# Optimization experiments

Measured on AMD Instinct MI355X. Metric: run time of the kernel, lower is better.

The kernel has to match this reference:

```python
import jax, jax.numpy as jnp
import numpy as np

N = 100000
E = 1600000
G = 2000
IN_C, HID, OUT = 9, 256, 128
BN_EPS = 1e-5


def setup_inputs() -> dict:
    key = jax.random.key(0)
    ks = jax.random.split(key, 12)
    x = jax.random.normal(ks[0], (N, IN_C), dtype=jnp.float32)
    edge_index = jax.random.randint(ks[1], (2, E), 0, N, dtype=jnp.int64)
    batch = jnp.sort(jax.random.randint(ks[2], (N,), 0, G, dtype=jnp.int64))
    # GCNConv weights (glorot-ish scale) and biases
    W1 = jax.random.normal(ks[3], (IN_C, HID), dtype=jnp.float32) * (1.0 / np.sqrt(IN_C))
    b1 = jnp.zeros((HID,), dtype=jnp.float32)
    W2 = jax.random.normal(ks[4], (HID, OUT), dtype=jnp.float32) * (1.0 / np.sqrt(HID))
    b2 = jnp.zeros((OUT,), dtype=jnp.float32)
    # BatchNorm affine params
    g1 = jnp.ones((HID,), dtype=jnp.float32)
    be1 = jnp.zeros((HID,), dtype=jnp.float32)
    g2 = jnp.ones((OUT,), dtype=jnp.float32)
    be2 = jnp.zeros((OUT,), dtype=jnp.float32)
    return {"x": x, "W1": W1, "b1": b1, "g1": g1, "be1": be1,
            "W2": W2, "b2": b2, "g2": g2, "be2": be2,
            "edge_index": edge_index, "batch": batch}


def _gcn_conv(x, W, b, src, dst, norm):
    # x: [N, F_in] -> [N, F_out]; PyG GCNConv: linear, then normalized scatter-add
    h = x @ W
    msg = h[src] * norm[:, None]                      # [E+N, F_out] edge messages
    out = jax.ops.segment_sum(msg, dst, num_segments=N)
    return out + b


def _batchnorm_train(h, gamma, beta):
    mean = jnp.mean(h, axis=0)
    var = jnp.mean(jnp.square(h - mean), axis=0)      # biased var, as torch BN
    return (h - mean) * jax.lax.rsqrt(var + BN_EPS) * gamma + beta


def reference(x, W1, b1, g1, be1, W2, b2, g2, be2, edge_index, batch):
    src, dst = edge_index[0], edge_index[1]
    loops = jnp.arange(N, dtype=src.dtype)
    src = jnp.concatenate([src, loops])               # add self-loops
    dst = jnp.concatenate([dst, loops])
    deg = jax.ops.segment_sum(jnp.ones_like(dst, dtype=x.dtype), dst, num_segments=N)
    dis = jax.lax.rsqrt(deg)                          # deg >= 1 due to self-loops
    norm = dis[src] * dis[dst]                        # symmetric normalization

    h = _gcn_conv(x, W1, b1, src, dst, norm)
    h = jax.nn.relu(_batchnorm_train(h, g1, be1))
    h = _gcn_conv(h, W2, b2, src, dst, norm)
    h = _batchnorm_train(h, g2, be2)

    # global mean pool over graphs
    sums = jax.ops.segment_sum(h, batch, num_segments=G)
    cnts = jax.ops.segment_sum(jnp.ones((N,), dtype=h.dtype), batch, num_segments=G)
    pooled = sums / jnp.maximum(cnts, 1.0)[:, None]

    # F.normalize(p=2, dim=1)
    nrm = jnp.linalg.norm(pooled, axis=1, keepdims=True)
    return pooled / jnp.maximum(nrm, 1e-12)
```

## Files before the change

kernel.cpp:

```cpp
#include <hip/hip_runtime.h>

#define N_NODES 100000
#define N_EDGES 1600000
#define N_GRAPH 2000
#define INC 9
#define HID 256
#define OUTC 128
#define BN_EPS 1e-5f
#define SCAN_CHUNK 1024
#define NSCAN ((N_NODES + SCAN_CHUNK - 1) / SCAN_CHUNK)
#define SP_NODES 64
#define SP_BLOCKS ((N_NODES + SP_NODES - 1) / SP_NODES)
#define NPART (2 * SP_BLOCKS)

typedef unsigned int uint;
typedef unsigned short ushort;
typedef short bf16x8 __attribute__((ext_vector_type(8)));
typedef float f32x4 __attribute__((ext_vector_type(4)));

static __device__ inline ushort f2bf(float f) {
    uint u = __float_as_uint(f);
    uint r = (u + 0x7fffu + ((u >> 16) & 1u)) >> 16;
    return (ushort)r;
}
static __device__ inline float bflo(uint p) { return __uint_as_float(p << 16); }
static __device__ inline float bfhi(uint p) { return __uint_as_float(p & 0xffff0000u); }


__global__ __launch_bounds__(256) void k_hist(const int* dst, int* degi, int* pose) {
    int e = blockIdx.x * 256 + threadIdx.x;
    if (e < N_EDGES) pose[e] = atomicAdd(&degi[dst[e]], 1);
}

__global__ __launch_bounds__(256) void k_scan1(const int* degi, int* exloc, int* bsum,
                                               float* dis) {
    __shared__ int s[SCAN_CHUNK];
    int t = threadIdx.x;
    int base = blockIdx.x * SCAN_CHUNK;
#pragma unroll
    for (int j = 0; j < 4; ++j) {
        int i = t + j * 256;
        int gi = base + i;
        int dv = (gi < N_NODES) ? degi[gi] : 0;
        s[i] = dv;
        if (gi < N_NODES) dis[gi] = rsqrtf((float)(dv + 1));
    }
    __syncthreads();
    for (int off = 1; off < SCAN_CHUNK; off <<= 1) {
        int v_[4];
#pragma unroll
        for (int j = 0; j < 4; ++j) {
            int i = t + j * 256;
            v_[j] = (i >= off) ? s[i - off] : 0;
        }
        __syncthreads();
#pragma unroll
        for (int j = 0; j < 4; ++j) s[t + j * 256] += v_[j];
        __syncthreads();
    }
#pragma unroll
    for (int j = 0; j < 4; ++j) {
        int i = t + j * 256;
        int gi = base + i;
        if (gi < N_NODES) exloc[gi] = i ? s[i - 1] : 0;
    }
    if (t == 0) bsum[blockIdx.x] = s[SCAN_CHUNK - 1];
}

__global__ void k_scan2(int* bsum) {
    if (threadIdx.x == 0 && blockIdx.x == 0) {
        int acc = 0;
        for (int i = 0; i < NSCAN; ++i) { int v = bsum[i]; bsum[i] = acc; acc += v; }
    }
}

__global__ __launch_bounds__(256) void k_scan3(const int* exloc, const int* bsum,
                                               int* row_start) {
    int v = blockIdx.x * 256 + threadIdx.x;
    if (v < N_NODES) row_start[v] = exloc[v] + bsum[v >> 10];
}

__global__ __launch_bounds__(256) void k_scatter(const int* src, const int* dst,
                                                 const float* dis, const int* row_start,
                                                 const int* pose, int2* csr) {
    int e = blockIdx.x * 256 + threadIdx.x;
    if (e < N_EDGES) {
        int s = src[e], d = dst[e];
        int pos = row_start[d] + pose[e];
        csr[pos] = make_int2(s, __float_as_int(dis[s] * dis[d]));
    }
}


__global__ __launch_bounds__(256) void k_w2t(const float* W2, ushort* W2Tg) {
    int i = blockIdx.x * 256 + threadIdx.x;
    if (i < HID * OUTC) {
        int col = i >> 8;
        int k = i & 255;
        W2Tg[i] = f2bf(W2[k * OUTC + col]);
    }
}


__global__ __launch_bounds__(256) void k_gather9(const float* x, const float* dis,
                                                 const int* row_start, const int* degi,
                                                 const int2* csr,
                                                 float* aggx) {
    int t = threadIdx.x;
    if (t >= 252) return;
    int v = blockIdx.x * 28 + t / 9;
    if (v >= N_NODES) return;
    int c = t % 9;
    float w = dis[v];
    float acc = w * w * x[v * INC + c];
    int r0 = row_start[v], dn = degi[v];
    for (int e = 0; e < dn; ++e) {
        int2 ed = csr[r0 + e];
        acc = fmaf(__int_as_float(ed.y), x[ed.x * INC + c], acc);
    }
    aggx[v * INC + c] = acc;
}


__global__ __launch_bounds__(256) void k_stats1(const float* aggx, const float* W1,
                                                double* stats) {
    __shared__ float sx[128][INC];
    int c = threadIdx.x;
    int v0 = blockIdx.x * 128;
    for (int i = threadIdx.x; i < 128 * INC; i += 256) {
        int vv = i / INC, cc = i % INC;
        int v = v0 + vv;
        sx[vv][cc] = (v < N_NODES) ? aggx[v * INC + cc] : 0.0f;
    }
    __syncthreads();
    float w[INC];
#pragma unroll
    for (int k = 0; k < INC; ++k) w[k] = W1[k * HID + c];
    double s = 0.0, s2 = 0.0;
    int nmax = min(128, N_NODES - v0);
    for (int n = 0; n < nmax; ++n) {
        float h = 0.0f;
#pragma unroll
        for (int k = 0; k < INC; ++k) h = fmaf(sx[n][k], w[k], h);
        s += (double)h;
        s2 += (double)h * (double)h;
    }
    atomicAdd(&stats[c], s);
    atomicAdd(&stats[HID + c], s2);
}

__global__ void k_finalize(const double* stats, const float* g, const float* be,
                           float* a, float* d, int C) {
    int c = blockIdx.x * blockDim.x + threadIdx.x;
    if (c < C) {
        const double invN = 1.0 / (double)N_NODES;
        float mean = (float)(stats[c] * invN);
        float ex2  = (float)(stats[C + c] * invN);
        float var  = ex2 - mean * mean;
        float istd = rsqrtf(var + BN_EPS);
        a[c] = istd * g[c];
        d[c] = be[c] - mean * istd * g[c];
    }
}


#define HPAD 88

__global__ __launch_bounds__(256) void k_gemm2_mfma(const float* aggx, const float* W1,
                                                    const ushort* W2Tg, const float* a1,
                                                    const float* d1, ushort* z) {
    __shared__ __align__(16) unsigned char smem[47616];
    ushort* sHb  = (ushort*)(smem);
    ushort* sW2T = (ushort*)(smem + 11264);
    float*  sW1f = (float*) (smem + 33792);
    float*  sA   = (float*) (smem + 43008);
    float*  sa1  = (float*) (smem + 45312);
    float*  sd1  = (float*) (smem + 46336);

    int t = threadIdx.x;
    int v0 = blockIdx.x * 64;

    for (int i = t; i < INC * HID; i += 256) sW1f[i] = W1[i];
    sa1[t] = a1[t & 255];
    sd1[t] = d1[t & 255];
    for (int i = t; i < 64 * INC; i += 256) {
        int vv = i / INC, cc = i % INC;
        int v = v0 + vv;
        sA[i] = (v < N_NODES) ? aggx[v * INC + cc] : 0.0f;
    }
    __syncthreads();

    int row = t >> 2, q = t & 3;
    int wave = t >> 6, lane = t & 63;
    int lr = lane & 15, lq = lane >> 4;

    float ax[INC];
#pragma unroll
    for (int k = 0; k < INC; ++k) ax[k] = sA[row * INC + k];

    f32x4 acc[8];
#pragma unroll
    for (int ct = 0; ct < 8; ++ct) acc[ct] = (f32x4){0.f, 0.f, 0.f, 0.f};

    for (int k0 = 0; k0 < HID; k0 += 64) {
#pragma unroll
        for (int i = 0; i < 4; ++i) {
            int idx = t + i * 256;
            int col = idx >> 3, sub = idx & 7;
            *(uint4*)&sW2T[col * HPAD + sub * 8] =
                *(const uint4*)&W2Tg[col * HID + k0 + sub * 8];
        }
#pragma unroll
        for (int jj = 0; jj < 8; ++jj) {
            int gc = k0 + q * 16 + jj * 2;
            float h0 = 0.f, h1 = 0.f;
#pragma unroll
            for (int k = 0; k < INC; ++k) {
                h0 = fmaf(ax[k], sW1f[k * HID + gc], h0);
                h1 = fmaf(ax[k], sW1f[k * HID + gc + 1], h1);
            }
            float hn0 = fmaxf(fmaf(h0, sa1[gc], sd1[gc]), 0.f);
            float hn1 = fmaxf(fmaf(h1, sa1[gc + 1], sd1[gc + 1]), 0.f);
            uint pk = (uint)f2bf(hn0) | ((uint)f2bf(hn1) << 16);
            *(uint*)&sHb[row * HPAD + q * 16 + jj * 2] = pk;
        }
        __syncthreads();
        int arow = (wave * 16 + lr) * HPAD + lq * 8;
        bf16x8 a0 = *(const bf16x8*)&sHb[arow];
        bf16x8 a1v = *(const bf16x8*)&sHb[arow + 32];
#pragma unroll
        for (int ct = 0; ct < 8; ++ct) {
            int brow = (ct * 16 + lr) * HPAD + lq * 8;
            bf16x8 b0 = *(const bf16x8*)&sW2T[brow];
            bf16x8 b1 = *(const bf16x8*)&sW2T[brow + 32];
            acc[ct] = __builtin_amdgcn_mfma_f32_16x16x32_bf16(a0, b0, acc[ct], 0, 0, 0);
            acc[ct] = __builtin_amdgcn_mfma_f32_16x16x32_bf16(a1v, b1, acc[ct], 0, 0, 0);
        }
        __syncthreads();
    }

    ushort* stage = (ushort*)smem;
#pragma unroll
    for (int ct = 0; ct < 8; ++ct)
#pragma unroll
        for (int r = 0; r < 4; ++r)
            stage[(wave * 16 + lq * 4 + r) * 128 + ct * 16 + lr] = f2bf(acc[ct][r]);
    __syncthreads();
#pragma unroll
    for (int i = 0; i < 4; ++i) {
        int idx = t + i * 256;
        int rr = idx >> 4, sub = idx & 15;
        int v = v0 + rr;
        if (v < N_NODES)
            *(uint4*)&z[(size_t)v * OUTC + sub * 8] =
                *(const uint4*)&stage[rr * 128 + sub * 8];
    }
}


__global__ __launch_bounds__(256) void k_gather128(const ushort* z, const float* dis,
                                                   const int* row_start, const int* degi,
                                                   const int2* csr,
                                                   float* agg2) {
    int t = threadIdx.x;
    int v = blockIdx.x * 16 + (t >> 4);
    if (v >= N_NODES) return;
    int c0 = (t & 15) * 8;

    float acc[8];
    float dv = dis[v];
    float w2 = dv * dv;
    uint4 zv = *(const uint4*)&z[(size_t)v * OUTC + c0];
    acc[0] = w2 * bflo(zv.x); acc[1] = w2 * bfhi(zv.x);
    acc[2] = w2 * bflo(zv.y); acc[3] = w2 * bfhi(zv.y);
    acc[4] = w2 * bflo(zv.z); acc[5] = w2 * bfhi(zv.z);
    acc[6] = w2 * bflo(zv.w); acc[7] = w2 * bfhi(zv.w);

    int r0 = row_start[v], dn = degi[v];
    for (int e = 0; e < dn; ++e) {
        int2 ed = csr[r0 + e];
        float ew = __int_as_float(ed.y);
        uint4 sv = *(const uint4*)&z[(size_t)ed.x * OUTC + c0];
        acc[0] = fmaf(ew, bflo(sv.x), acc[0]);
        acc[1] = fmaf(ew, bfhi(sv.x), acc[1]);
        acc[2] = fmaf(ew, bflo(sv.y), acc[2]);
        acc[3] = fmaf(ew, bfhi(sv.y), acc[3]);
        acc[4] = fmaf(ew, bflo(sv.z), acc[4]);
        acc[5] = fmaf(ew, bfhi(sv.z), acc[5]);
        acc[6] = fmaf(ew, bflo(sv.w), acc[6]);
        acc[7] = fmaf(ew, bfhi(sv.w), acc[7]);
    }
    float4 lo = make_float4(acc[0], acc[1], acc[2], acc[3]);
    float4 hi = make_float4(acc[4], acc[5], acc[6], acc[7]);
    *(float4*)&agg2[(size_t)v * OUTC + c0] = lo;
    *(float4*)&agg2[(size_t)v * OUTC + c0 + 4] = hi;
}


__global__ __launch_bounds__(256) void k_stats_pool(const float* agg2, const int* batch,
                                                    double* part, float* psum, float* pcnt) {
    int t = threadIdx.x;
    int c = t & 127;
    int half = t >> 7;
    int p = blockIdx.x * 2 + half;
    int v0 = blockIdx.x * SP_NODES + half * (SP_NODES / 2);
    double s = 0.0, s2 = 0.0;
    if (v0 < N_NODES) {
        int vend = min(v0 + SP_NODES / 2, N_NODES);
        float acc = 0.0f;
        int cnt = 0;
        int gprev = batch[v0];
        for (int v = v0; v < vend; ++v) {
            float h = agg2[(size_t)v * OUTC + c];
            s += (double)h;
            s2 += (double)h * (double)h;
            int g = batch[v];
            if (g != gprev) {
                atomicAdd(&psum[gprev * OUTC + c], acc);
                if (c == 0) atomicAdd(&pcnt[gprev], (float)cnt);
                acc = 0.0f; cnt = 0; gprev = g;
            }
            acc += h;
            cnt++;
        }
        atomicAdd(&psum[gprev * OUTC + c], acc);
        if (c == 0) atomicAdd(&pcnt[gprev], (float)cnt);
    }
    part[(size_t)p * 256 + c]       = s;
    part[(size_t)p * 256 + 128 + c] = s2;
}

__global__ __launch_bounds__(256) void k_stats_red(const double* part, double* stats) {
    __shared__ double red[256];
    int t = threadIdx.x;
    int slot = blockIdx.x;
    double s = 0.0;
    for (int p = t; p < NPART; p += 256) s += part[(size_t)p * 256 + slot];
    red[t] = s;
    __syncthreads();
    for (int o = 128; o > 0; o >>= 1) {
        if (t < o) red[t] += red[t + o];
        __syncthreads();
    }
    if (t == 0) stats[slot] = red[0];
}


__global__ __launch_bounds__(128) void k_out(const float* psum, const float* pcnt,
                                             const float* a2, const float* d2,
                                             float* out) {
    int g = blockIdx.x;
    int c = threadIdx.x;
    float cnt = fmaxf(pcnt[g], 1.0f);
    float m = fmaf(psum[g * OUTC + c] / cnt, a2[c], d2[c]);
    float ss = m * m;
#pragma unroll
    for (int o = 1; o < 64; o <<= 1) ss += __shfl_xor(ss, o);
    __shared__ float ws[2];
    if ((c & 63) == 0) ws[c >> 6] = ss;
    __syncthreads();
    float nrm = sqrtf(ws[0] + ws[1]);
    out[g * OUTC + c] = m / fmaxf(nrm, 1e-12f);
}


extern "C" void kernel_launch(void* const* d_in, const int* in_sizes, int n_in,
                              void* d_out, int out_size, void* d_ws, size_t ws_size,
                              hipStream_t stream) {
    const float* x   = (const float*)d_in[0];
    const float* W1  = (const float*)d_in[1];
    const float* g1  = (const float*)d_in[3];
    const float* be1 = (const float*)d_in[4];
    const float* W2  = (const float*)d_in[5];
    const float* g2  = (const float*)d_in[7];
    const float* be2 = (const float*)d_in[8];
    const int* ei    = (const int*)d_in[9];
    const int* batch = (const int*)d_in[10];
    const int* src = ei;
    const int* dst = ei + N_EDGES;
    float* out = (float*)d_out;

    char* ws = (char*)d_ws;
    size_t off = 0;
    auto alloc = [&](size_t b) {
        char* p = ws + off;
        off = (off + b + 255) & ~(size_t)255;
        return p;
    };
    float*  dis   = (float*)alloc((size_t)N_NODES * 4);
    int*    degi  = (int*)  alloc((size_t)N_NODES * 4);
    int*    pose  = (int*)  alloc((size_t)N_EDGES * 4);
    int*    exloc = (int*)  alloc((size_t)N_NODES * 4);
    int*    rowst = (int*)  alloc((size_t)N_NODES * 4);
    int*    bsum  = (int*)  alloc((size_t)NSCAN * 4);
    int2*   csr   = (int2*) alloc((size_t)N_EDGES * 8);
    float*  aggx  = (float*)alloc((size_t)N_NODES * INC * 4);
    ushort* z     = (ushort*)alloc((size_t)N_NODES * OUTC * 2);
    ushort* w2t   = (ushort*)alloc((size_t)HID * OUTC * 2);
    float*  agg2  = (float*)alloc((size_t)N_NODES * OUTC * 4);
    double* part  = (double*)alloc((size_t)NPART * 256 * 8);
    double* st1   = (double*)alloc(2 * HID * 8);
    double* st2   = (double*)alloc(2 * OUTC * 8);
    float*  a1    = (float*)alloc(HID * 4);
    float*  d1    = (float*)alloc(HID * 4);
    float*  a2    = (float*)alloc(OUTC * 4);
    float*  d2    = (float*)alloc(OUTC * 4);
    float*  psum  = (float*)alloc((size_t)N_GRAPH * OUTC * 4);
    float*  pcnt  = (float*)alloc((size_t)N_GRAPH * 4);

    hipMemsetAsync(degi, 0, (size_t)N_NODES * 4, stream);
    hipMemsetAsync(st1, 0, 2 * HID * 8, stream);
    hipMemsetAsync(psum, 0, (size_t)N_GRAPH * OUTC * 4, stream);
    hipMemsetAsync(pcnt, 0, (size_t)N_GRAPH * 4, stream);

    k_hist<<<(N_EDGES + 255) / 256, 256, 0, stream>>>(dst, degi, pose);
    k_scan1<<<NSCAN, 256, 0, stream>>>(degi, exloc, bsum, dis);
    k_scan2<<<1, 64, 0, stream>>>(bsum);
    k_scan3<<<(N_NODES + 255) / 256, 256, 0, stream>>>(exloc, bsum, rowst);
    k_scatter<<<(N_EDGES + 255) / 256, 256, 0, stream>>>(src, dst, dis, rowst, pose, csr);
    k_w2t<<<(HID * OUTC + 255) / 256, 256, 0, stream>>>(W2, w2t);
    k_gather9<<<(N_NODES + 27) / 28, 256, 0, stream>>>(x, dis, rowst, degi, csr, aggx);
    k_stats1<<<(N_NODES + 127) / 128, 256, 0, stream>>>(aggx, W1, st1);
    k_finalize<<<1, HID, 0, stream>>>(st1, g1, be1, a1, d1, HID);
    k_gemm2_mfma<<<(N_NODES + 63) / 64, 256, 0, stream>>>(aggx, W1, w2t, a1, d1, z);
    k_gather128<<<(N_NODES + 15) / 16, 256, 0, stream>>>(z, dis, rowst, degi, csr, agg2);
    k_stats_pool<<<SP_BLOCKS, 256, 0, stream>>>(agg2, batch, part, psum, pcnt);
    k_stats_red<<<256, 256, 0, stream>>>(part, st2);
    k_finalize<<<1, OUTC, 0, stream>>>(st2, g2, be2, a2, d2, OUTC);
    k_out<<<N_GRAPH, OUTC, 0, stream>>>(psum, pcnt, a2, d2, out);
}
```

Baseline: 393.0 us.

## Fuse 9-channel gather with BN1 stats and use chunked partial reductions

Merges the first-layer neighbor gather and the BN1 statistics pass into one kernel. Each block keeps its 28 aggregated nodes in shared memory and writes per-block double partials instead of issuing global atomics. A new generic chunked reducer (32 blocks, each summing a range of partials and then atomically adding) replaces the old one-block-per-slot tree reduction, and it is also used for the BN2 stats. This removes a kernel launch, a global re-read of aggx and contended double atomics. In exchange it adds a large partial buffer (about 3572 blocks × 512 doubles) and a separate reduction pass.

```diff
diff --git a/kernel.cpp b/kernel.cpp
--- a/kernel.cpp
+++ b/kernel.cpp
@@ -12,6 +12,8 @@
 #define SP_NODES 64
 #define SP_BLOCKS ((N_NODES + SP_NODES - 1) / SP_NODES)
 #define NPART (2 * SP_BLOCKS)
+#define G9_NODES 28
+#define G9_BLOCKS ((N_NODES + G9_NODES - 1) / G9_NODES)
 
 typedef unsigned int uint;
 typedef unsigned short ushort;
@@ -102,42 +104,38 @@
 }
 
 
-__global__ __launch_bounds__(256) void k_gather9(const float* x, const float* dis,
-                                                 const int* row_start, const int* degi,
-                                                 const int2* csr,
-                                                 float* aggx) {
-    int t = threadIdx.x;
-    if (t >= 252) return;
-    int v = blockIdx.x * 28 + t / 9;
-    if (v >= N_NODES) return;
-    int c = t % 9;
-    float w = dis[v];
-    float acc = w * w * x[v * INC + c];
-    int r0 = row_start[v], dn = degi[v];
-    for (int e = 0; e < dn; ++e) {
-        int2 ed = csr[r0 + e];
-        acc = fmaf(__int_as_float(ed.y), x[ed.x * INC + c], acc);
-    }
-    aggx[v * INC + c] = acc;
-}
-
-
-__global__ __launch_bounds__(256) void k_stats1(const float* aggx, const float* W1,
-                                                double* stats) {
-    __shared__ float sx[128][INC];
-    int c = threadIdx.x;
-    int v0 = blockIdx.x * 128;
-    for (int i = threadIdx.x; i < 128 * INC; i += 256) {
-        int vv = i / INC, cc = i % INC;
-        int v = v0 + vv;
-        sx[vv][cc] = (v < N_NODES) ? aggx[v * INC + cc] : 0.0f;
+__global__ __launch_bounds__(256) void k_gather9s(const float* x, const float* dis,
+                                                  const int* row_start, const int* degi,
+                                                  const int2* csr, const float* W1,
+                                                  float* aggx, double* part1) {
+    __shared__ float sx[G9_NODES][INC];
+    int t = threadIdx.x;
+    int b = blockIdx.x;
+    int v0 = b * G9_NODES;
+
+    if (t < G9_NODES * INC) {
+        int v = v0 + t / INC;
+        if (v < N_NODES) {
+            int c = t % INC;
+            float w = dis[v];
+            float acc = w * w * x[v * INC + c];
+            int r0 = row_start[v], dn = degi[v];
+            for (int e = 0; e < dn; ++e) {
+                int2 ed = csr[r0 + e];
+                acc = fmaf(__int_as_float(ed.y), x[ed.x * INC + c], acc);
+            }
+            aggx[v * INC + c] = acc;
+            sx[t / INC][c] = acc;
+        }
     }
     __syncthreads();
+
+    int c = t;
     float w[INC];
 #pragma unroll
     for (int k = 0; k < INC; ++k) w[k] = W1[k * HID + c];
     double s = 0.0, s2 = 0.0;
-    int nmax = min(128, N_NODES - v0);
+    int nmax = min(G9_NODES, N_NODES - v0);
     for (int n = 0; n < nmax; ++n) {
         float h = 0.0f;
 #pragma unroll
@@ -145,8 +143,20 @@
         s += (double)h;
         s2 += (double)h * (double)h;
     }
-    atomicAdd(&stats[c], s);
-    atomicAdd(&stats[HID + c], s2);
+    part1[(size_t)b * 512 + c]       = s;
+    part1[(size_t)b * 512 + 256 + c] = s2;
+}
+
+__global__ __launch_bounds__(256) void k_red(const double* part, double* stats,
+                                             int npart, int nslots, int chunk) {
+    int t = threadIdx.x;
+    int p0 = blockIdx.x * chunk;
+    int pe = min(p0 + chunk, npart);
+    for (int s = t; s < nslots; s += 256) {
+        double acc = 0.0;
+        for (int p = p0; p < pe; ++p) acc += part[(size_t)p * nslots + s];
+        atomicAdd(&stats[s], acc);
+    }
 }
 
 __global__ void k_finalize(const double* stats, const float* g, const float* be,
@@ -330,21 +340,6 @@
     part[(size_t)p * 256 + 128 + c] = s2;
 }
 
-__global__ __launch_bounds__(256) void k_stats_red(const double* part, double* stats) {
-    __shared__ double red[256];
-    int t = threadIdx.x;
-    int slot = blockIdx.x;
-    double s = 0.0;
-    for (int p = t; p < NPART; p += 256) s += part[(size_t)p * 256 + slot];
-    red[t] = s;
-    __syncthreads();
-    for (int o = 128; o > 0; o >>= 1) {
-        if (t < o) red[t] += red[t + o];
-        __syncthreads();
-    }
-    if (t == 0) stats[slot] = red[0];
-}
-
 
 __global__ __launch_bounds__(128) void k_out(const float* psum, const float* pcnt,
                                              const float* a2, const float* d2,
@@ -399,6 +394,7 @@
     ushort* w2t   = (ushort*)alloc((size_t)HID * OUTC * 2);
     float*  agg2  = (float*)alloc((size_t)N_NODES * OUTC * 4);
     double* part  = (double*)alloc((size_t)NPART * 256 * 8);
+    double* part1 = (double*)alloc((size_t)G9_BLOCKS * 512 * 8);
     double* st1   = (double*)alloc(2 * HID * 8);
     double* st2   = (double*)alloc(2 * OUTC * 8);
     float*  a1    = (float*)alloc(HID * 4);
@@ -410,6 +406,7 @@
 
     hipMemsetAsync(degi, 0, (size_t)N_NODES * 4, stream);
     hipMemsetAsync(st1, 0, 2 * HID * 8, stream);
+    hipMemsetAsync(st2, 0, 2 * OUTC * 8, stream);
     hipMemsetAsync(psum, 0, (size_t)N_GRAPH * OUTC * 4, stream);
     hipMemsetAsync(pcnt, 0, (size_t)N_GRAPH * 4, stream);
 
@@ -419,13 +416,13 @@
     k_scan3<<<(N_NODES + 255) / 256, 256, 0, stream>>>(exloc, bsum, rowst);
     k_scatter<<<(N_EDGES + 255) / 256, 256, 0, stream>>>(src, dst, dis, rowst, pose, csr);
     k_w2t<<<(HID * OUTC + 255) / 256, 256, 0, stream>>>(W2, w2t);
-    k_gather9<<<(N_NODES + 27) / 28, 256, 0, stream>>>(x, dis, rowst, degi, csr, aggx);
-    k_stats1<<<(N_NODES + 127) / 128, 256, 0, stream>>>(aggx, W1, st1);
+    k_gather9s<<<G9_BLOCKS, 256, 0, stream>>>(x, dis, rowst, degi, csr, W1, aggx, part1);
+    k_red<<<32, 256, 0, stream>>>(part1, st1, G9_BLOCKS, 512, (G9_BLOCKS + 31) / 32);
     k_finalize<<<1, HID, 0, stream>>>(st1, g1, be1, a1, d1, HID);
     k_gemm2_mfma<<<(N_NODES + 63) / 64, 256, 0, stream>>>(aggx, W1, w2t, a1, d1, z);
     k_gather128<<<(N_NODES + 15) / 16, 256, 0, stream>>>(z, dis, rowst, degi, csr, agg2);
     k_stats_pool<<<SP_BLOCKS, 256, 0, stream>>>(agg2, batch, part, psum, pcnt);
-    k_stats_red<<<256, 256, 0, stream>>>(part, st2);
+    k_red<<<32, 256, 0, stream>>>(part, st2, NPART, 256, (NPART + 31) / 32);
     k_finalize<<<1, OUTC, 0, stream>>>(st2, g2, be2, a2, d2, OUTC);
     k_out<<<N_GRAPH, OUTC, 0, stream>>>(psum, pcnt, a2, d2, out);
 }
```

Result: slower. 453.6 us (+15.4%).
